# Performance work log

Measured on AMD Instinct MI355X. Metric: run time of the kernel, lower is better.

The kernel has to match this reference:

```python
import jax, jax.numpy as jnp
import numpy as np

B, S, D = 4, 4096, 1024
H, WIN = 16, 256
DK = D // H
NW = S // WIN


def setup_inputs() -> dict:
    key = jax.random.key(0)
    ks = jax.random.split(key, 11)
    mk = lambda k, shape: jax.random.normal(k, shape, dtype=jnp.float32)
    w = lambda k: mk(k, (D, D)) * 0.02  # torch Linear weight [out, in]
    b = lambda k: mk(k, (D,)) * 0.02
    return {
        "query": mk(ks[0], (B, S, D)),
        "key": mk(ks[1], (B, S, D)),
        "value": mk(ks[2], (B, S, D)),
        "Wq": w(ks[3]), "bq": b(ks[4]),
        "Wk": w(ks[5]), "bk": b(ks[6]),
        "Wv": w(ks[7]), "bv": b(ks[8]),
        "Wo": w(ks[9]), "bo": b(ks[10]),
    }


def reference(query, key, value, Wq, bq, Wk, bk, Wv, bv, Wo, bo):
    scale = 1.0 / float(DK) ** 0.5

    def proj(x, Wm, bi):
        y = x @ Wm.T + bi
        return y.reshape(B, S, H, DK).transpose(0, 2, 1, 3).reshape(B, H, NW, WIN, DK)

    q = proj(query, Wq, bq)
    k = proj(key, Wk, bk)
    v = proj(value, Wv, bv)

    scores = jnp.einsum("bhnqd,bhnkd->bhnqk", q, k) * scale
    p_attn = jax.nn.softmax(scores, axis=-1)
    x = jnp.einsum("bhnqk,bhnkd->bhnqd", p_attn, v)

    # merge windows + heads -> [B,S,D], then output projection
    x = x.reshape(B, H, S, DK).transpose(0, 2, 1, 3).reshape(B, S, D)
    return x @ Wo.T + bo
```

## Files before the change

### kernel.cpp

```cpp
#include <hip/hip_runtime.h>
#include <hip/hip_bf16.h>

typedef __attribute__((ext_vector_type(8))) __bf16 bf16x8;
typedef __attribute__((ext_vector_type(4))) float f32x4;

#define DEVI static __device__ __forceinline__


DEVI ushort f2bf(float f) {
  unsigned u = __builtin_bit_cast(unsigned, f);
  return (ushort)((u + 0x7fffu + ((u >> 16) & 1u)) >> 16);
}

union BF8 { unsigned u[4]; bf16x8 v; };

DEVI bf16x8 cvt8(const float* __restrict__ p) {
  const f32x4 a = *(const f32x4*)p;
  const f32x4 b = *(const f32x4*)(p + 4);
  BF8 r;
  asm("v_cvt_pk_bf16_f32 %0, %1, %2" : "=v"(r.u[0]) : "v"(a.x), "v"(a.y));
  asm("v_cvt_pk_bf16_f32 %0, %1, %2" : "=v"(r.u[1]) : "v"(a.z), "v"(a.w));
  asm("v_cvt_pk_bf16_f32 %0, %1, %2" : "=v"(r.u[2]) : "v"(b.x), "v"(b.y));
  asm("v_cvt_pk_bf16_f32 %0, %1, %2" : "=v"(r.u[3]) : "v"(b.z), "v"(b.w));
  return r.v;
}

DEVI bf16x8 cvt8r(f32x4 a, f32x4 b) {
  BF8 r;
  asm("v_cvt_pk_bf16_f32 %0, %1, %2" : "=v"(r.u[0]) : "v"(a.x), "v"(a.y));
  asm("v_cvt_pk_bf16_f32 %0, %1, %2" : "=v"(r.u[1]) : "v"(a.z), "v"(a.w));
  asm("v_cvt_pk_bf16_f32 %0, %1, %2" : "=v"(r.u[2]) : "v"(b.x), "v"(b.y));
  asm("v_cvt_pk_bf16_f32 %0, %1, %2" : "=v"(r.u[3]) : "v"(b.z), "v"(b.w));
  return r.v;
}

DEVI unsigned cvtpk1(float lo, float hi) {
  unsigned r;
  asm("v_cvt_pk_bf16_f32 %0, %1, %2" : "=v"(r) : "v"(lo), "v"(hi));
  return r;
}

DEVI void gload16(const void* g, void* l) {
  __builtin_amdgcn_global_load_lds(
      (const __attribute__((address_space(1))) unsigned*)g,
      (__attribute__((address_space(3))) unsigned*)l, 16, 0, 0);
}

DEVI int xcd_swizzle(int bid, int nwg) {
  return (bid & 7) * (nwg >> 3) + (bid >> 3);
}

DEVI f32x4 mfma16(bf16x8 a, bf16x8 b, f32x4 c) {
  return __builtin_amdgcn_mfma_f32_16x16x32_bf16(a, b, c, 0, 0, 0);
}


__global__ __launch_bounds__(256) void cvt_w(
    const float* __restrict__ wq, const float* __restrict__ wk,
    const float* __restrict__ wv, const float* __restrict__ wo,
    ushort* __restrict__ oq, ushort* __restrict__ ok2,
    ushort* __restrict__ ov, ushort* __restrict__ oo) {
  const int s = blockIdx.x >> 7;
  const int tb = blockIdx.x & 127;
  const float* src = s == 0 ? wq : (s == 1 ? wk : (s == 2 ? wv : wo));
  ushort* dst = s == 0 ? oq : (s == 1 ? ok2 : (s == 2 ? ov : oo));
  const unsigned G = 128 * 256;
  const unsigned t = tb * 256 + threadIdx.x;
#pragma unroll
  for (int j = 0; j < 4; ++j) {
    const size_t i = (size_t)t + (size_t)j * G;
    *(bf16x8*)(dst + i * 8) = cvt8(src + i * 8);
  }
}


template <int OUT>
__global__ __launch_bounds__(512, 2) void gemm_8ph(
    const ushort* __restrict__ A, const ushort* __restrict__ B,
    const float* __restrict__ bias, void* __restrict__ Cp, int N, int K) {
  __shared__ __align__(16) ushort Asm[4][8192];
  __shared__ __align__(16) ushort Bsm[4][8192];
  const int tid = threadIdx.x, lane = tid & 63;
  const int wv = tid >> 6;
  const int wr = wv >> 2, wc = wv & 3;
  const int cc = lane & 15, cr = lane >> 4;
  const int nw = N >> 8;
  const int work = xcd_swizzle(blockIdx.x, gridDim.x);
  const size_t m0 = (size_t)(work / nw) * 256;
  const size_t n0 = (size_t)(work % nw) * 256;

  const ushort *ag[2], *bg[2];
#pragma unroll
  for (int h = 0; h < 2; ++h) {
    const int u = tid + h * 512;
    const int row = u >> 2, slot = u & 3;
    const int gc = (slot ^ ((row >> 1) & 3)) * 8;
    ag[h] = A + (m0 + row) * (size_t)K + gc;
    bg[h] = B + (n0 + row) * (size_t)K + gc;
  }

  auto stageh = [&](int buf, int kt, int h) {
    gload16(ag[h] + kt, &Asm[buf][(tid + h * 512) * 8]);
    gload16(bg[h] + kt, &Bsm[buf][(tid + h * 512) * 8]);
  };

  f32x4 acc[8][4] = {};
  const int nt = K >> 5;

  int aoff[8], boff[4];
#pragma unroll
  for (int m = 0; m < 8; ++m) {
    const int row = wr * 128 + m * 16 + cc;
    aoff[m] = (row * 4 + (cr ^ ((row >> 1) & 3))) * 8;
  }
#pragma unroll
  for (int n = 0; n < 4; ++n) {
    const int row = wc * 64 + n * 16 + cc;
    boff[n] = (row * 4 + (cr ^ ((row >> 1) & 3))) * 8;
  }

#pragma unroll
  for (int p = 0; p < 3; ++p) {
    stageh(p, p << 5, 0);
    stageh(p, p << 5, 1);
  }
  asm volatile("s_waitcnt vmcnt(8)" ::: "memory");
  __builtin_amdgcn_s_barrier();
  asm volatile("" ::: "memory");

  for (int k = 0; k < nt; ++k) {
    const ushort* Ab = Asm[k & 3];
    const ushort* Bb = Bsm[k & 3];
    const int wb = (k + 3) & 3;
    const bool more = (k + 3 < nt);
    bf16x8 bf[4], af[4];

#pragma unroll
    for (int n = 0; n < 4; ++n) bf[n] = *(const bf16x8*)&Bb[boff[n]];
#pragma unroll
    for (int m = 0; m < 4; ++m) af[m] = *(const bf16x8*)&Ab[aoff[m]];
    if (more) stageh(wb, (k + 3) << 5, 0);
    __builtin_amdgcn_s_barrier();
    asm volatile("s_waitcnt lgkmcnt(0)" ::: "memory");
    __builtin_amdgcn_s_setprio(1);
#pragma unroll
    for (int m = 0; m < 4; ++m)
#pragma unroll
      for (int n = 0; n < 4; ++n)
        acc[m][n] = mfma16(af[m], bf[n], acc[m][n]);
    __builtin_amdgcn_s_setprio(0);
    asm volatile("" ::: "memory");
    __builtin_amdgcn_s_barrier();

#pragma unroll
    for (int m = 0; m < 4; ++m) af[m] = *(const bf16x8*)&Ab[aoff[4 + m]];
    if (more) stageh(wb, (k + 3) << 5, 1);
    if (k < nt - 3) {
      asm volatile("s_waitcnt vmcnt(8)" ::: "memory");
    } else if (k == nt - 3) {
      asm volatile("s_waitcnt vmcnt(4)" ::: "memory");
    } else if (k == nt - 2) {
      asm volatile("s_waitcnt vmcnt(0)" ::: "memory");
    }
    __builtin_amdgcn_s_barrier();
    asm volatile("s_waitcnt lgkmcnt(0)" ::: "memory");
    __builtin_amdgcn_s_setprio(1);
#pragma unroll
    for (int m = 0; m < 4; ++m)
#pragma unroll
      for (int n = 0; n < 4; ++n)
        acc[4 + m][n] = mfma16(af[m], bf[n], acc[4 + m][n]);
    __builtin_amdgcn_s_setprio(0);
    asm volatile("" ::: "memory");
    __builtin_amdgcn_s_barrier();
  }

#pragma unroll
  for (int n = 0; n < 4; ++n) {
    const size_t col = n0 + wc * 64 + n * 16 + cc;
    const float bval = bias[col];
#pragma unroll
    for (int m = 0; m < 8; ++m) {
      const size_t row0 = m0 + wr * 128 + m * 16 + cr * 4;
#pragma unroll
      for (int r = 0; r < 4; ++r) {
        const float val = acc[m][n][r] + bval;
        if constexpr (OUT == 0)
          ((float*)Cp)[(row0 + r) * N + col] = val;
        else if constexpr (OUT == 1)
          ((ushort*)Cp)[(row0 + r) * N + col] = f2bf(val);
        else
          ((ushort*)Cp)[col * 16384 + row0 + r] = f2bf(val);
      }
    }
  }
}


template <int OUT>
__global__ __launch_bounds__(512, 2) void gemm_8ph_f32a(
    const float* __restrict__ A, const ushort* __restrict__ B,
    const float* __restrict__ bias, void* __restrict__ Cp, int N, int K) {
  __shared__ __align__(16) ushort Asm[4][8192];
  __shared__ __align__(16) ushort Bsm[4][8192];
  const int tid = threadIdx.x, lane = tid & 63;
  const int wv = tid >> 6;
  const int wr = wv >> 2, wc = wv & 3;
  const int cc = lane & 15, cr = lane >> 4;
  const int nw = N >> 8;
  const int work = xcd_swizzle(blockIdx.x, gridDim.x);
  const size_t m0 = (size_t)(work / nw) * 256;
  const size_t n0 = (size_t)(work % nw) * 256;

  const float *af0, *af1;
  ushort *al0, *al1;
  {
    const int u0 = tid, r0 = u0 >> 2, s0 = u0 & 3;
    const int u1 = tid + 512, r1 = u1 >> 2, s1 = u1 & 3;
    af0 = A + (m0 + r0) * (size_t)K + (s0 ^ ((r0 >> 1) & 3)) * 8;
    af1 = A + (m0 + r1) * (size_t)K + (s1 ^ ((r1 >> 1) & 3)) * 8;
    al0 = &Asm[0][0] + u0 * 8;
    al1 = &Asm[0][0] + u1 * 8;
  }
  const ushort* bg[2];
#pragma unroll
  for (int h = 0; h < 2; ++h) {
    const int u = tid + h * 512;
    const int row = u >> 2, slot = u & 3;
    bg[h] = B + (n0 + row) * (size_t)K + (slot ^ ((row >> 1) & 3)) * 8;
  }

  f32x4 acc[8][4] = {};
  const int nt = K >> 5;

  int aoff[8], boff[4];
#pragma unroll
  for (int m = 0; m < 8; ++m) {
    const int row = wr * 128 + m * 16 + cc;
    aoff[m] = (row * 4 + (cr ^ ((row >> 1) & 3))) * 8;
  }
#pragma unroll
  for (int n = 0; n < 4; ++n) {
    const int row = wc * 64 + n * 16 + cc;
    boff[n] = (row * 4 + (cr ^ ((row >> 1) & 3))) * 8;
  }

  f32x4 sa0, sa1, sa2, sa3, sb0, sb1, sb2, sb3;
#pragma unroll
  for (int p = 0; p < 2; ++p) {
    const int kt = p << 5;
    sa0 = *(const f32x4*)(af0 + kt);  sa1 = *(const f32x4*)(af0 + kt + 4);
    sa2 = *(const f32x4*)(af1 + kt);  sa3 = *(const f32x4*)(af1 + kt + 4);
    *(bf16x8*)(al0 + p * 8192) = cvt8r(sa0, sa1);
    *(bf16x8*)(al1 + p * 8192) = cvt8r(sa2, sa3);
  }
  sa0 = *(const f32x4*)(af0 + 64);  sa1 = *(const f32x4*)(af0 + 68);
  sa2 = *(const f32x4*)(af1 + 64);  sa3 = *(const f32x4*)(af1 + 68);
#pragma unroll
  for (int p = 0; p < 3; ++p) {
    gload16(bg[0] + (p << 5), &Bsm[p][tid * 8]);
    gload16(bg[1] + (p << 5), &Bsm[p][(tid + 512) * 8]);
  }
  asm volatile("s_waitcnt vmcnt(0) lgkmcnt(0)" ::: "memory");
  __builtin_amdgcn_s_barrier();
  asm volatile("" ::: "memory");

#define F32A_TILE(k, W0, W1, W2, W3, L0, L1, L2, L3)                          \
  {                                                                           \
    const ushort* Ab = Asm[(k) & 3];                                          \
    const ushort* Bb = Bsm[(k) & 3];                                          \
    const int wb = ((k) + 3) & 3;                                             \
    const bool more = ((k) + 3 < nt);                                         \
    bf16x8 bf[4], af[4];                                                      \
    _Pragma("unroll")                                                         \
    for (int n = 0; n < 4; ++n) bf[n] = *(const bf16x8*)&Bb[boff[n]];         \
    _Pragma("unroll")                                                         \
    for (int m = 0; m < 4; ++m) af[m] = *(const bf16x8*)&Ab[aoff[m]];         \
    if ((k) + 2 < nt) { \
      const int wbuf = ((k) + 2) & 3;                                         \
      *(bf16x8*)(al0 + wbuf * 8192) = cvt8r(W0, W1);                          \
      *(bf16x8*)(al1 + wbuf * 8192) = cvt8r(W2, W3);                          \
    }                                                                         \
    if (more) {                                                               \
      const int kt = ((k) + 3) << 5;                                          \
      L0 = *(const f32x4*)(af0 + kt);  L1 = *(const f32x4*)(af0 + kt + 4);    \
      L2 = *(const f32x4*)(af1 + kt);  L3 = *(const f32x4*)(af1 + kt + 4);    \
      gload16(bg[0] + kt, &Bsm[wb][tid * 8]);                                 \
    }                                                                         \
    if ((k) < nt - 3) {                                                       \
      asm volatile("s_waitcnt vmcnt(17)" ::: "memory");                       \
    } else if ((k) == nt - 3) {                                               \
      asm volatile("s_waitcnt vmcnt(12)" ::: "memory");                       \
    } else if ((k) == nt - 2) {                                               \
      asm volatile("s_waitcnt vmcnt(6)" ::: "memory");                        \
    } else {                                                                  \
      asm volatile("s_waitcnt vmcnt(0)" ::: "memory");                        \
    }                                                                         \
    __builtin_amdgcn_s_barrier();                                             \
    asm volatile("s_waitcnt lgkmcnt(0)" ::: "memory");                        \
    __builtin_amdgcn_s_setprio(1);                                            \
    _Pragma("unroll")                                                         \
    for (int m = 0; m < 4; ++m)                                               \
      _Pragma("unroll")                                                       \
      for (int n = 0; n < 4; ++n) acc[m][n] = mfma16(af[m], bf[n], acc[m][n]);\
    __builtin_amdgcn_s_setprio(0);                                            \
    asm volatile("" ::: "memory");                                            \
    __builtin_amdgcn_s_barrier();                                             \
    _Pragma("unroll")                                                         \
    for (int m = 0; m < 4; ++m) af[m] = *(const bf16x8*)&Ab[aoff[4 + m]];     \
    if (more) gload16(bg[1] + (((k) + 3) << 5), &Bsm[wb][(tid + 512) * 8]);   \
    __builtin_amdgcn_s_barrier();                                             \
    asm volatile("s_waitcnt lgkmcnt(0)" ::: "memory");                        \
    __builtin_amdgcn_s_setprio(1);                                            \
    _Pragma("unroll")                                                         \
    for (int m = 0; m < 4; ++m)                                               \
      _Pragma("unroll")                                                       \
      for (int n = 0; n < 4; ++n)                                             \
        acc[4 + m][n] = mfma16(af[m], bf[n], acc[4 + m][n]);                  \
    __builtin_amdgcn_s_setprio(0);                                            \
    asm volatile("" ::: "memory");                                            \
    __builtin_amdgcn_s_barrier();                                             \
  }

  for (int kk = 0; kk < nt; kk += 2) {
    F32A_TILE(kk, sa0, sa1, sa2, sa3, sb0, sb1, sb2, sb3);
    F32A_TILE(kk + 1, sb0, sb1, sb2, sb3, sa0, sa1, sa2, sa3);
  }
#undef F32A_TILE

#pragma unroll
  for (int n = 0; n < 4; ++n) {
    const size_t col = n0 + wc * 64 + n * 16 + cc;
    const float bval = bias[col];
#pragma unroll
    for (int m = 0; m < 8; ++m) {
      const size_t row0 = m0 + wr * 128 + m * 16 + cr * 4;
#pragma unroll
      for (int r = 0; r < 4; ++r) {
        const float val = acc[m][n][r] + bval;
        if constexpr (OUT == 1)
          ((ushort*)Cp)[(row0 + r) * N + col] = f2bf(val);
        else
          ((ushort*)Cp)[col * 16384 + row0 + r] = f2bf(val);
      }
    }
  }
}


__global__ __launch_bounds__(512) void attn_kernel(
    const ushort* __restrict__ q, const ushort* __restrict__ k,
    const ushort* __restrict__ vt, ushort* __restrict__ x) {
  __shared__ __align__(16) ushort Ks[256 * 64];
  __shared__ __align__(16) ushort Vt[64 * 256];
  __shared__ ushort Pw[8][16 * 264];
  const int bid = blockIdx.x;
  const int w = bid & 15, h = (bid >> 4) & 15, b = bid >> 8;
  const int tid = threadIdx.x, lane = tid & 63, wv = tid >> 6;
  const int cc = lane & 15, cr = lane >> 4;
  const size_t base = ((size_t)b * 4096 + (size_t)w * 256) * 1024 + h * 64;
  const size_t vbase = ((size_t)h * 64) * 16384 + (size_t)b * 4096 + w * 256;

  const ushort* qp0 = q + base + (size_t)(wv * 32 + cc) * 1024 + cr * 8;
  const ushort* qp1 = q + base + (size_t)(wv * 32 + 16 + cc) * 1024 + cr * 8;
  const bf16x8 qA0 = *(const bf16x8*)qp0;
  const bf16x8 qA1 = *(const bf16x8*)(qp0 + 32);
  const bf16x8 qB0 = *(const bf16x8*)qp1;
  const bf16x8 qB1 = *(const bf16x8*)(qp1 + 32);

#pragma unroll
  for (int i = 0; i < 4; ++i) {
    const int u = tid + i * 512;
    const int row = u >> 3, slot = u & 7;
    gload16(k + base + (size_t)row * 1024 + ((slot ^ (row & 7)) << 3),
            &Ks[u * 8]);
  }
#pragma unroll
  for (int i = 0; i < 4; ++i) {
    const int u = tid + i * 512;
    const int dk = u >> 5, slot = u & 31;
    gload16(vt + vbase + (size_t)dk * 16384 + (((slot & 24) | ((slot ^ dk) & 7)) << 3),
            &Vt[u * 8]);
  }
  __syncthreads();

  ushort* Pp = Pw[wv];
  for (int c = 0; c < 2; ++c) {
    const int qrow0 = wv * 32 + c * 16;
    const bf16x8 qf0 = c == 0 ? qA0 : qB0;
    const bf16x8 qf1 = c == 0 ? qA1 : qB1;

    f32x4 sc[16];
    __builtin_amdgcn_s_setprio(1);
#pragma unroll
    for (int cb = 0; cb < 16; ++cb) {
      const int row = cb * 16 + cc;
      const bf16x8 kb0 = *(const bf16x8*)&Ks[row * 64 + ((cr ^ (row & 7)) << 3)];
      const bf16x8 kb1 =
          *(const bf16x8*)&Ks[row * 64 + (((4 + cr) ^ (row & 7)) << 3)];
      f32x4 z = {0.f, 0.f, 0.f, 0.f};
      z = mfma16(qf0, kb0, z);
      z = mfma16(qf1, kb1, z);
      sc[cb] = z;
    }
    __builtin_amdgcn_s_setprio(0);

    float inv[4];
#pragma unroll
    for (int r = 0; r < 4; ++r) {
      float mx = -1e30f;
#pragma unroll
      for (int cb = 0; cb < 16; ++cb) mx = fmaxf(mx, sc[cb][r]);
      mx = fmaxf(mx, __shfl_xor(mx, 1));
      mx = fmaxf(mx, __shfl_xor(mx, 2));
      mx = fmaxf(mx, __shfl_xor(mx, 4));
      mx = fmaxf(mx, __shfl_xor(mx, 8));
      float sum = 0.f;
#pragma unroll
      for (int cb = 0; cb < 16; ++cb) {
        const float p = __expf((sc[cb][r] - mx) * 0.125f);
        sc[cb][r] = p;
        sum += p;
      }
      sum += __shfl_xor(sum, 1);
      sum += __shfl_xor(sum, 2);
      sum += __shfl_xor(sum, 4);
      sum += __shfl_xor(sum, 8);
      inv[r] = 1.f / sum;
    }

#pragma unroll
    for (int r = 0; r < 4; ++r) {
      ushort* prow = &Pp[(cr * 4 + r) * 264 + cc];
#pragma unroll
      for (int cb = 0; cb < 16; cb += 2) {
        const unsigned pk = cvtpk1(sc[cb][r], sc[cb + 1][r]);
        prow[cb * 16] = (ushort)pk;
        prow[(cb + 1) * 16] = (ushort)(pk >> 16);
      }
    }

    bf16x8 pf[8];
#pragma unroll
    for (int ks = 0; ks < 8; ++ks)
      pf[ks] = *(const bf16x8*)&Pp[cc * 264 + ks * 32 + cr * 8];
    f32x4 o[4] = {};
    __builtin_amdgcn_s_setprio(1);
#pragma unroll
    for (int db = 0; db < 4; ++db) {
      const int row = db * 16 + cc;
#pragma unroll
      for (int ks = 0; ks < 8; ++ks) {
        const int gu = ks * 4 + cr;
        const int lu = (gu & 24) | ((gu ^ row) & 7);
        const bf16x8 bv = *(const bf16x8*)&Vt[row * 256 + lu * 8];
        o[db] = mfma16(pf[ks], bv, o[db]);
      }
    }
    __builtin_amdgcn_s_setprio(0);

#pragma unroll
    for (int db = 0; db < 4; ++db)
#pragma unroll
      for (int r = 0; r < 4; ++r) {
        const int qr = qrow0 + cr * 4 + r;
        x[base + (size_t)qr * 1024 + db * 16 + cc] = f2bf(o[db][r] * inv[r]);
      }
  }
}


extern "C" void kernel_launch(void* const* d_in, const int* in_sizes, int n_in,
                              void* d_out, int out_size, void* d_ws, size_t ws_size,
                              hipStream_t stream) {
  const float* query = (const float*)d_in[0];
  const float* key_  = (const float*)d_in[1];
  const float* value = (const float*)d_in[2];
  const float* Wq = (const float*)d_in[3];
  const float* bq = (const float*)d_in[4];
  const float* Wk = (const float*)d_in[5];
  const float* bk = (const float*)d_in[6];
  const float* Wv = (const float*)d_in[7];
  const float* bv = (const float*)d_in[8];
  const float* Wo = (const float*)d_in[9];
  const float* bo = (const float*)d_in[10];
  float* out = (float*)d_out;

  const size_t MN = (size_t)16384 * 1024;
  const size_t WN = (size_t)1024 * 1024;
  ushort* wqb = (ushort*)d_ws;
  ushort* wkb = wqb + WN;
  ushort* wvb = wkb + WN;
  ushort* wob = wvb + WN;
  ushort* qp = wob + WN;
  ushort* kp = qp + MN;
  ushort* vtp = kp + MN;

  const dim3 b256(256), b512(512);
  const dim3 ggrid(256);

  cvt_w<<<dim3(4 * 128), b256, 0, stream>>>(Wq, Wk, Wv, Wo, wqb, wkb, wvb, wob);

  gemm_8ph_f32a<1><<<ggrid, b512, 0, stream>>>(query, wqb, bq, qp, 1024, 1024);
  gemm_8ph_f32a<1><<<ggrid, b512, 0, stream>>>(key_,  wkb, bk, kp, 1024, 1024);
  gemm_8ph_f32a<2><<<ggrid, b512, 0, stream>>>(value, wvb, bv, vtp, 1024, 1024);

  attn_kernel<<<dim3(1024), b512, 0, stream>>>(qp, kp, vtp, qp );

  gemm_8ph<0><<<ggrid, b512, 0, stream>>>(qp, wob, bo, out, 1024, 1024);
}
```

Before: 268.8 us.

## Read V directly from global memory and split P staging into two halves

Drops the shared-memory staging of the transposed V tile in the attention kernel. The PV MFMAs now read V fragments straight from global memory (L2-cached), and the P matrix is written to LDS in two 128-column halves, which shrinks the per-wave P buffer. The lower LDS footprint is meant to raise occupancy and remove the V copy-in. In exchange, V is re-read from global memory by every wave, adding global load latency inside the MFMA loop, and with no sync between the P store and the P read on the same wave buffer there may be a hazard across the halves.

```diff
diff --git a/kernel.cpp b/kernel.cpp
--- a/kernel.cpp
+++ b/kernel.cpp
@@ -276,7 +276,7 @@
     for (int n = 0; n < 4; ++n) bf[n] = *(const bf16x8*)&Bb[boff[n]];         \
     _Pragma("unroll")                                                         \
     for (int m = 0; m < 4; ++m) af[m] = *(const bf16x8*)&Ab[aoff[m]];         \
-    if ((k) + 2 < nt) { \
+    if ((k) + 2 < nt) {                                                       \
       const int wbuf = ((k) + 2) & 3;                                         \
       *(bf16x8*)(al0 + wbuf * 8192) = cvt8r(W0, W1);                          \
       *(bf16x8*)(al1 + wbuf * 8192) = cvt8r(W2, W3);                          \
@@ -352,8 +352,7 @@
     const ushort* __restrict__ q, const ushort* __restrict__ k,
     const ushort* __restrict__ vt, ushort* __restrict__ x) {
   __shared__ __align__(16) ushort Ks[256 * 64];
-  __shared__ __align__(16) ushort Vt[64 * 256];
-  __shared__ ushort Pw[8][16 * 264];
+  __shared__ ushort Pw[8][16 * 136];
   const int bid = blockIdx.x;
   const int w = bid & 15, h = (bid >> 4) & 15, b = bid >> 8;
   const int tid = threadIdx.x, lane = tid & 63, wv = tid >> 6;
@@ -374,13 +373,6 @@
     const int row = u >> 3, slot = u & 7;
     gload16(k + base + (size_t)row * 1024 + ((slot ^ (row & 7)) << 3),
             &Ks[u * 8]);
-  }
-#pragma unroll
-  for (int i = 0; i < 4; ++i) {
-    const int u = tid + i * 512;
-    const int dk = u >> 5, slot = u & 31;
-    gload16(vt + vbase + (size_t)dk * 16384 + (((slot & 24) | ((slot ^ dk) & 7)) << 3),
-            &Vt[u * 8]);
   }
   __syncthreads();
 
@@ -429,35 +421,37 @@
       inv[r] = 1.f / sum;
     }
 
-#pragma unroll
-    for (int r = 0; r < 4; ++r) {
-      ushort* prow = &Pp[(cr * 4 + r) * 264 + cc];
-#pragma unroll
-      for (int cb = 0; cb < 16; cb += 2) {
-        const unsigned pk = cvtpk1(sc[cb][r], sc[cb + 1][r]);
-        prow[cb * 16] = (ushort)pk;
-        prow[(cb + 1) * 16] = (ushort)(pk >> 16);
+    f32x4 o[4] = {};
+#pragma unroll
+    for (int ph = 0; ph < 2; ++ph) {
+#pragma unroll
+      for (int r = 0; r < 4; ++r) {
+        ushort* prow = &Pp[(cr * 4 + r) * 136 + cc];
+#pragma unroll
+        for (int cb0 = 0; cb0 < 8; cb0 += 2) {
+          const unsigned pk =
+              cvtpk1(sc[ph * 8 + cb0][r], sc[ph * 8 + cb0 + 1][r]);
+          prow[cb0 * 16] = (ushort)pk;
+          prow[(cb0 + 1) * 16] = (ushort)(pk >> 16);
+        }
       }
+      bf16x8 pf[4];
+#pragma unroll
+      for (int j = 0; j < 4; ++j)
+        pf[j] = *(const bf16x8*)&Pp[cc * 136 + j * 32 + cr * 8];
+      __builtin_amdgcn_s_setprio(1);
+#pragma unroll
+      for (int db = 0; db < 4; ++db) {
+        const ushort* vrow = vt + vbase + (size_t)(db * 16 + cc) * 16384;
+#pragma unroll
+        for (int j = 0; j < 4; ++j) {
+          const int gu = (ph * 4 + j) * 4 + cr;
+          const bf16x8 bv = *(const bf16x8*)(vrow + gu * 8);
+          o[db] = mfma16(pf[j], bv, o[db]);
+        }
+      }
+      __builtin_amdgcn_s_setprio(0);
     }
-
-    bf16x8 pf[8];
-#pragma unroll
-    for (int ks = 0; ks < 8; ++ks)
-      pf[ks] = *(const bf16x8*)&Pp[cc * 264 + ks * 32 + cr * 8];
-    f32x4 o[4] = {};
-    __builtin_amdgcn_s_setprio(1);
-#pragma unroll
-    for (int db = 0; db < 4; ++db) {
-      const int row = db * 16 + cc;
-#pragma unroll
-      for (int ks = 0; ks < 8; ++ks) {
-        const int gu = ks * 4 + cr;
-        const int lu = (gu & 24) | ((gu ^ row) & 7);
-        const bf16x8 bv = *(const bf16x8*)&Vt[row * 256 + lu * 8];
-        o[db] = mfma16(pf[ks], bv, o[db]);
-      }
-    }
-    __builtin_amdgcn_s_setprio(0);
 
 #pragma unroll
     for (int db = 0; db < 4; ++db)
```

New measurement: 344.1 us. 1.28x slower.
